# Performance work log

Measured on AMD Instinct MI355X. Metric: run time of the kernel, lower is better.

The kernel has to match this reference:

```python
import jax, jax.numpy as jnp
import numpy as np

B, N, C, L = 32, 1024, 1024, 16  # batch, pixels (HW), channels, visual tokens


def setup_inputs() -> dict:
    key = jax.random.key(0)
    ks = jax.random.split(key, 18)
    s = lambda fan_in: 1.0 / np.sqrt(fan_in)
    def lin(kw, kb, fin, fout):
        W = jax.random.uniform(kw, (fin, fout), jnp.float32, -s(fin), s(fin))
        b = jax.random.uniform(kb, (fout,), jnp.float32, -s(fin), s(fin))
        return W, b
    tok_W, tok_b = lin(ks[0], ks[1], C, L)          # tokenizer pointwise conv
    key_W, key_b = lin(ks[2], ks[3], C, C // 2)     # transformer key proj
    query_W, query_b = lin(ks[4], ks[5], C, C // 2) # transformer query proj
    f1_W, f1_b = lin(ks[6], ks[7], C, C)            # FFN 1
    f2_W, f2_b = lin(ks[8], ks[9], C, C)            # FFN 2
    q_W, q_b = lin(ks[10], ks[11], C, C)            # projector W_q
    k_W, k_b = lin(ks[12], ks[13], C, C)            # projector W_k
    feature_map = jax.random.normal(ks[14], (B, N, C), jnp.float32)
    T_in = jnp.zeros((B, L, C), jnp.float32)  # unused by FilterBasedTokenizer
    return dict(feature_map=feature_map, T_in=T_in,
                tok_W=tok_W, tok_b=tok_b, key_W=key_W, key_b=key_b,
                query_W=query_W, query_b=query_b, f1_W=f1_W, f1_b=f1_b,
                f2_W=f2_W, f2_b=f2_b, q_W=q_W, q_b=q_b, k_W=k_W, k_b=k_b)


def reference(feature_map, T_in, tok_W, tok_b, key_W, key_b, query_W, query_b,
              f1_W, f1_b, f2_W, f2_b, q_W, q_b, k_W, k_b):
    X = feature_map  # [B, N, C]
    # --- FilterBasedTokenizer: softmax over pixel dim, aggregate pixels -> tokens
    proj = X @ tok_W + tok_b                         # [B, N, L]
    attn = jax.nn.softmax(proj, axis=1)              # softmax over N (dim=1)
    T = jnp.einsum('bnl,bnc->blc', attn, X)          # [B, L, C]
    # --- Transformer block on visual tokens
    k = T @ key_W + key_b                            # [B, L, C/2]
    q = T @ query_W + query_b                        # [B, L, C/2]
    scores = jnp.einsum('bld,bmd->blm', k, q)        # [B, L, L]
    T_dash = T + jax.nn.softmax(scores, axis=2) @ T  # self-attn residual
    T_out = T_dash + (jax.nn.relu(T_dash @ f1_W + f1_b) @ f2_W + f2_b)
    # --- Projector: pixels attend to tokens
    sim = jnp.einsum('bnc,blc->bnl', X @ q_W + q_b, T_out @ k_W + k_b)  # [B, N, L]
    X_out = X + jax.nn.softmax(sim, axis=2) @ T_out  # [B, N, C]
    return (X_out, T_out)
```

## Files before the change

kernel.cpp:

```cpp
#include <hip/hip_runtime.h>
#include <hip/hip_bf16.h>
#include <stdint.h>

#define BB 32
#define NN 1024
#define CC 1024
#define LL 16

typedef __attribute__((ext_vector_type(4))) float f32x4;
typedef __attribute__((ext_vector_type(8))) short short8;
typedef __attribute__((ext_vector_type(4))) unsigned short ushort4v;

__device__ __forceinline__ unsigned short f2bf(float f) {
  union { float f; unsigned u; } v; v.f = f;
  unsigned r = v.u + 0x7FFF + ((v.u >> 16) & 1);
  return (unsigned short)(r >> 16);
}
__device__ __forceinline__ float bf2f(unsigned short h) {
  union { unsigned u; float f; } v; v.u = ((unsigned)h) << 16; return v.f;
}
__device__ __forceinline__ short8 cvt8(f32x4 a, f32x4 b) {
  short8 r;
  r[0] = (short)f2bf(a[0]); r[1] = (short)f2bf(a[1]);
  r[2] = (short)f2bf(a[2]); r[3] = (short)f2bf(a[3]);
  r[4] = (short)f2bf(b[0]); r[5] = (short)f2bf(b[1]);
  r[6] = (short)f2bf(b[2]); r[7] = (short)f2bf(b[3]);
  return r;
}

__global__ __launch_bounds__(256) void wprep(
    const float* __restrict__ keyW, const float* __restrict__ queryW,
    const float* __restrict__ f1W, const float* __restrict__ f2W,
    const float* __restrict__ kW, const float* __restrict__ qW,
    const float* __restrict__ tokW, const float* __restrict__ keyb,
    const float* __restrict__ queryb,
    unsigned short* __restrict__ WkqT, unsigned short* __restrict__ f1WT,
    unsigned short* __restrict__ f2WT, unsigned short* __restrict__ kWT,
    unsigned short* __restrict__ qWbf, unsigned short* __restrict__ tokWT,
    float* __restrict__ biaskq)
{
  int z = blockIdx.z;
  int tx = threadIdx.x, ty = threadIdx.y;
  if (z == 5) {
    int gid = (blockIdx.y * 32 + blockIdx.x) * 256 + ty * 32 + tx;
    if (gid < 16384) {
      int l = gid >> 10, c = gid & 1023;
      tokWT[gid] = f2bf(tokW[c * 16 + l]);
    } else if (gid < 17408) {
      int i = gid - 16384;
      biaskq[i] = (i < 512) ? keyb[i] : queryb[i - 512];
    }
    return;
  }
  if (z == 4) {
#pragma unroll
    for (int i = 0; i < 4; ++i) {
      int row = blockIdx.y * 32 + ty + 8 * i;
      int col = blockIdx.x * 32 + tx;
      qWbf[row * 1024 + col] = f2bf(qW[row * 1024 + col]);
    }
    return;
  }
  __shared__ float tile[32][33];
  int j0 = blockIdx.x * 32, k0 = blockIdx.y * 32;
  const float* src = (z == 1) ? f1W : (z == 2) ? f2W : kW;
#pragma unroll
  for (int i = 0; i < 4; ++i) {
    int k = k0 + ty + 8 * i;
    int j = j0 + tx;
    float v;
    if (z == 0) v = (j < 512) ? keyW[k * 512 + j] : queryW[k * 512 + (j - 512)];
    else        v = src[k * 1024 + j];
    tile[ty + 8 * i][tx] = v;
  }
  __syncthreads();
  unsigned short* dst = (z == 0) ? WkqT : (z == 1) ? f1WT : (z == 2) ? f2WT : kWT;
#pragma unroll
  for (int i = 0; i < 4; ++i) {
    int j = j0 + ty + 8 * i;
    dst[j * 1024 + k0 + tx] = f2bf(tile[tx][ty + 8 * i]);
  }
}

__global__ __launch_bounds__(256) void tok_fused(
    const float* __restrict__ X, const unsigned short* __restrict__ tokWT,
    const float* __restrict__ tokB, unsigned short* __restrict__ Tp,
    float* __restrict__ Mloc, float* __restrict__ Sloc)
{
  __shared__ float E[64][16];
  __shared__ float redm[4][16];
  __shared__ float reds[4][16];
  int tid = threadIdx.x, wid = tid >> 6, lane = tid & 63;
  int lr = lane & 15, hi = lane >> 4;
  int b = blockIdx.y, ch = blockIdx.x;
  int pix0 = b * 1024 + ch * 64;
  const float* Ar = X + (size_t)(pix0 + wid * 16 + lr) * 1024 + hi * 8;
  const unsigned short* Br = tokWT + lr * 1024 + hi * 8;
  f32x4 acc = (f32x4)0.f;
#pragma unroll 8
  for (int k0 = 0; k0 < 1024; k0 += 32) {
    f32x4 x0 = *(const f32x4*)(Ar + k0);
    f32x4 x1 = *(const f32x4*)(Ar + k0 + 4);
    short8 bfrag = *(const short8*)(Br + k0);
    acc = __builtin_amdgcn_mfma_f32_16x16x32_bf16(cvt8(x0, x1), bfrag, acc, 0, 0, 0);
  }
  float tb = tokB[lr];
  float sv[4];
#pragma unroll
  for (int rr = 0; rr < 4; ++rr) sv[rr] = acc[rr] + tb;
  float pm = fmaxf(fmaxf(sv[0], sv[1]), fmaxf(sv[2], sv[3]));
  pm = fmaxf(pm, __shfl_xor(pm, 16));
  pm = fmaxf(pm, __shfl_xor(pm, 32));
  if (hi == 0) redm[wid][lr] = pm;
  __syncthreads();
  float m = fmaxf(fmaxf(redm[0][lr], redm[1][lr]), fmaxf(redm[2][lr], redm[3][lr]));
  float ev[4]; float ps = 0.f;
#pragma unroll
  for (int i = 0; i < 4; ++i) { ev[i] = __expf(sv[i] - m); ps += ev[i]; }
  ps += __shfl_xor(ps, 16); ps += __shfl_xor(ps, 32);
  if (hi == 0) reds[wid][lr] = ps;
#pragma unroll
  for (int rr = 0; rr < 4; ++rr)
    E[wid * 16 + hi * 4 + rr][lr] = ev[rr];
  __syncthreads();
  if (tid < 16) {
    float sl = reds[0][tid] + reds[1][tid] + reds[2][tid] + reds[3][tid];
    Mloc[(b * 16 + ch) * 16 + tid] = m;
    Sloc[(b * 16 + ch) * 16 + tid] = sl;
  }
  f32x4 a16[16];
#pragma unroll
  for (int l = 0; l < 16; ++l) a16[l] = (f32x4)0.f;
  const float* xp = X + (size_t)pix0 * 1024 + tid * 4;
  for (int n0 = 0; n0 < 64; n0 += 8) {
    f32x4 xv[8];
#pragma unroll
    for (int i = 0; i < 8; ++i) xv[i] = *(const f32x4*)(xp + (size_t)(n0 + i) * 1024);
#pragma unroll
    for (int i = 0; i < 8; ++i) {
      const f32x4* ar = (const f32x4*)&E[n0 + i][0];
      f32x4 a0 = ar[0], a1 = ar[1], a2 = ar[2], a3 = ar[3];
      f32x4 x0 = xv[i];
      a16[0]  += a0[0]*x0; a16[1]  += a0[1]*x0; a16[2]  += a0[2]*x0; a16[3]  += a0[3]*x0;
      a16[4]  += a1[0]*x0; a16[5]  += a1[1]*x0; a16[6]  += a1[2]*x0; a16[7]  += a1[3]*x0;
      a16[8]  += a2[0]*x0; a16[9]  += a2[1]*x0; a16[10] += a2[2]*x0; a16[11] += a2[3]*x0;
      a16[12] += a3[0]*x0; a16[13] += a3[1]*x0; a16[14] += a3[2]*x0; a16[15] += a3[3]*x0;
    }
  }
  unsigned short* op = Tp + ((size_t)(b * 16 + ch) * 16) * 1024 + tid * 4;
#pragma unroll
  for (int l = 0; l < 16; ++l) {
    f32x4 s = a16[l];
    ushort4v h; h[0]=f2bf(s[0]); h[1]=f2bf(s[1]); h[2]=f2bf(s[2]); h[3]=f2bf(s[3]);
    *(ushort4v*)(op + (size_t)l * 1024) = h;
  }
}

__global__ __launch_bounds__(256) void tmerge(
    const unsigned short* __restrict__ Tp, const float* __restrict__ Mloc,
    const float* __restrict__ Sloc, float* __restrict__ T,
    unsigned short* __restrict__ Tbf)
{
  int tid = threadIdx.x;
  int g = blockIdx.x * 2 + (tid >> 7);
  int b = g >> 4, l = g & 15;
  int j = tid & 127;
  float M = -1e30f;
#pragma unroll
  for (int ch = 0; ch < 16; ++ch) M = fmaxf(M, Mloc[(b * 16 + ch) * 16 + l]);
  float w[16]; float denom = 0.f;
#pragma unroll
  for (int ch = 0; ch < 16; ++ch) {
    w[ch] = __expf(Mloc[(b * 16 + ch) * 16 + l] - M);
    denom += w[ch] * Sloc[(b * 16 + ch) * 16 + l];
  }
  float inv = 1.f / denom;
  float o[8];
#pragma unroll
  for (int t = 0; t < 8; ++t) o[t] = 0.f;
#pragma unroll
  for (int ch = 0; ch < 16; ++ch) {
    const unsigned short* p = Tp + ((size_t)((b * 16 + ch) * 16 + l)) * 1024 + j * 8;
    short8 v = *(const short8*)p;
    float wc = w[ch];
#pragma unroll
    for (int t = 0; t < 8; ++t) o[t] += wc * bf2f((unsigned short)v[t]);
  }
  f32x4 o0, o1; short8 hb;
#pragma unroll
  for (int t = 0; t < 4; ++t) {
    float x0 = o[t] * inv, x1 = o[4 + t] * inv;
    o0[t] = x0; o1[t] = x1;
    hb[t] = (short)f2bf(x0); hb[4 + t] = (short)f2bf(x1);
  }
  *(f32x4*)(T + (size_t)g * 1024 + j * 8) = o0;
  *(f32x4*)(T + (size_t)g * 1024 + j * 8 + 4) = o1;
  *(short8*)(Tbf + (size_t)g * 1024 + j * 8) = hb;
}

template<int RELU, int HAS_BIAS, int HAS_RES, int STORE_F32, int STORE_BF16>
__global__ __launch_bounds__(256) void gemm32x64(
    const unsigned short* __restrict__ A, const unsigned short* __restrict__ Bm,
    const float* __restrict__ bias, const float* __restrict__ res,
    float* __restrict__ outF, unsigned short* __restrict__ outB)
{
  const int K = 1024;
  __shared__ __align__(16) char sh[12288];
  char* Asp = sh;
  char* Bsp = sh + 4096;
  int tid = threadIdx.x, wid = tid >> 6, lane = tid & 63;
  int lr = lane & 15, hi = lane >> 4;
  int m0 = blockIdx.x * 32, n0 = blockIdx.y * 64;
  int arow = tid >> 3, acol = (tid & 7) * 8;
  int brow = tid >> 2, bcol = (tid & 3) * 16;
  const unsigned short* Ap = A + (size_t)(m0 + arow) * K + acol;
  const unsigned short* Bp = Bm + (size_t)(n0 + brow) * K + bcol;
  int aw  = arow * 128 + (((acol * 2) ^ ((arow & 7) << 4)));
  int bw0 = brow * 128 + (((bcol * 2) ^ ((brow & 7) << 4)));
  int bw1 = brow * 128 + ((((bcol * 2) + 16) ^ ((brow & 7) << 4)));
  short8 aR[2]; short8 bR[2][2];
  aR[0]    = *(const short8*)(Ap);
  bR[0][0] = *(const short8*)(Bp);
  bR[0][1] = *(const short8*)(Bp + 8);
  aR[1]    = *(const short8*)(Ap + 64);
  bR[1][0] = *(const short8*)(Bp + 64);
  bR[1][1] = *(const short8*)(Bp + 72);
  f32x4 acc[2];
  acc[0] = (f32x4)0.f; acc[1] = (f32x4)0.f;
  int wm = (wid >> 1) * 16, wn = (wid & 1) * 32;
  int arb = (wm + lr) * 128, arx = ((wm + lr) & 7) << 4;
  for (int s = 0; s < 16; ++s) {
    __syncthreads();
    *(short8*)(Asp + aw)  = aR[s & 1];
    *(short8*)(Bsp + bw0) = bR[s & 1][0];
    *(short8*)(Bsp + bw1) = bR[s & 1][1];
    __syncthreads();
    if (s + 2 < 16) {
      int k0 = (s + 2) * 64;
      aR[s & 1]    = *(const short8*)(Ap + k0);
      bR[s & 1][0] = *(const short8*)(Bp + k0);
      bR[s & 1][1] = *(const short8*)(Bp + k0 + 8);
    }
#pragma unroll
    for (int kk = 0; kk < 2; ++kk) {
      short8 af = *(const short8*)(Asp + arb + (((kk * 64 + hi * 16) ^ arx)));
#pragma unroll
      for (int sn = 0; sn < 2; ++sn) {
        int br = wn + sn * 16 + lr;
        short8 bf = *(const short8*)(Bsp + br * 128 + (((kk * 64 + hi * 16) ^ ((br & 7) << 4))));
        acc[sn] = __builtin_amdgcn_mfma_f32_16x16x32_bf16(af, bf, acc[sn], 0, 0, 0);
      }
    }
  }
  int row0 = m0 + wm + hi * 4;
#pragma unroll
  for (int sn = 0; sn < 2; ++sn) {
    int col = n0 + wn + sn * 16 + lr;
    float bv_ = HAS_BIAS ? bias[col] : 0.f;
#pragma unroll
    for (int rr = 0; rr < 4; ++rr) {
      float x = acc[sn][rr] + bv_;
      if (RELU) x = fmaxf(x, 0.f);
      size_t idx = (size_t)(row0 + rr) * 1024 + col;
      if (HAS_RES) x += res[idx];
      if (STORE_F32) outF[idx] = x;
      if (STORE_BF16) outB[idx] = f2bf(x);
    }
  }
}

__global__ __launch_bounds__(256) void scores_tdash(
    const float* __restrict__ kq, const float* __restrict__ T,
    float* __restrict__ Tdash, unsigned short* __restrict__ Tdbf)
{
  int cs = blockIdx.x, b = blockIdx.y;
  int c0 = cs * 128;
  __shared__ float Ts[16][128];
  int tid = threadIdx.x, lane = tid & 63;
#pragma unroll
  for (int i = 0; i < 2; ++i) {
    int fi = tid + 256 * i;
    int rrow = fi >> 5, c4 = (fi & 31) * 4;
    *(f32x4*)&Ts[rrow][c4] = *(const f32x4*)&T[((size_t)b * 16 + rrow) * 1024 + c0 + c4];
  }
  __syncthreads();
  int l = tid >> 4, m = tid & 15;
  const float* krow = kq + ((size_t)b * 16 + l) * 1024;
  const float* qrow = kq + ((size_t)b * 16 + m) * 1024 + 512;
  float s = 0.f;
#pragma unroll 8
  for (int d = 0; d < 512; d += 4) {
    f32x4 kv = *(const f32x4*)(krow + d);
    f32x4 qv = *(const f32x4*)(qrow + d);
    s += kv[0]*qv[0] + kv[1]*qv[1] + kv[2]*qv[2] + kv[3]*qv[3];
  }
  float mx = s;
  mx = fmaxf(mx, __shfl_xor(mx, 1)); mx = fmaxf(mx, __shfl_xor(mx, 2));
  mx = fmaxf(mx, __shfl_xor(mx, 4)); mx = fmaxf(mx, __shfl_xor(mx, 8));
  float e = __expf(s - mx);
  float sum = e;
  sum += __shfl_xor(sum, 1); sum += __shfl_xor(sum, 2);
  sum += __shfl_xor(sum, 4); sum += __shfl_xor(sum, 8);
  float pv = e / sum;
  float pl[16];
#pragma unroll
  for (int i = 0; i < 16; ++i) pl[i] = __shfl(pv, (lane & 48) + i);
  float* od = Tdash + ((size_t)b * 16 + l) * 1024 + c0;
  unsigned short* ob = Tdbf + ((size_t)b * 16 + l) * 1024 + c0;
#pragma unroll
  for (int h = 0; h < 2; ++h) {
    int c = m * 8 + h * 4;
    f32x4 o = *(const f32x4*)&Ts[l][c];
#pragma unroll
    for (int mm = 0; mm < 16; ++mm) {
      f32x4 tv = *(const f32x4*)&Ts[mm][c];
      o += pl[mm] * tv;
    }
    *(f32x4*)(od + c) = o;
    ushort4v hh; hh[0]=f2bf(o[0]); hh[1]=f2bf(o[1]); hh[2]=f2bf(o[2]); hh[3]=f2bf(o[3]);
    *(ushort4v*)(ob + c) = hh;
  }
}

__global__ __launch_bounds__(256) void r_kernel(
    const unsigned short* __restrict__ Tkbf, const float* __restrict__ qb,
    float* __restrict__ r)
{
  int row = blockIdx.x * 4 + (threadIdx.x >> 6);
  int lane = threadIdx.x & 63;
  const unsigned short* p = Tkbf + (size_t)row * CC;
  float s = 0.f;
#pragma unroll
  for (int h = 0; h < 2; ++h) {
    int d0 = lane * 8 + h * 512;
    short8 v = *(const short8*)&p[d0];
#pragma unroll
    for (int jj = 0; jj < 8; ++jj)
      s += bf2f((unsigned short)v[jj]) * qb[d0 + jj];
  }
#pragma unroll
  for (int msk = 32; msk >= 1; msk >>= 1) s += __shfl_xor(s, msk);
  if (lane == 0) r[row] = s;
}

__global__ __launch_bounds__(256) void sim_out_kernel(
    const float* __restrict__ X, const unsigned short* __restrict__ Gt,
    const float* __restrict__ rbias, const float* __restrict__ Tout,
    float* __restrict__ Xout)
{
  __shared__ float Ps[64][16];
  int tid = threadIdx.x, wid = tid >> 6, lane = tid & 63;
  int lr = lane & 15, hi = lane >> 4;
  int b = blockIdx.y;
  int pix0 = b * 1024 + blockIdx.x * 64;
  const float* Ar = X + (size_t)(pix0 + wid * 16 + lr) * 1024 + hi * 8;
  const unsigned short* Br = Gt + (size_t)b * 16384 + lr * 1024 + hi * 8;
  f32x4 acc = (f32x4)0.f;
#pragma unroll 8
  for (int k0 = 0; k0 < 1024; k0 += 32) {
    f32x4 x0 = *(const f32x4*)(Ar + k0);
    f32x4 x1 = *(const f32x4*)(Ar + k0 + 4);
    short8 bfrag = *(const short8*)(Br + k0);
    acc = __builtin_amdgcn_mfma_f32_16x16x32_bf16(cvt8(x0, x1), bfrag, acc, 0, 0, 0);
  }
  float bv = rbias[b * 16 + lr];
  int prow = wid * 16 + hi * 4;
#pragma unroll
  for (int rr = 0; rr < 4; ++rr) {
    float vv = acc[rr] + bv;
    float mx = vv;
    mx = fmaxf(mx, __shfl_xor(mx, 1)); mx = fmaxf(mx, __shfl_xor(mx, 2));
    mx = fmaxf(mx, __shfl_xor(mx, 4)); mx = fmaxf(mx, __shfl_xor(mx, 8));
    float e = __expf(vv - mx);
    float ss = e;
    ss += __shfl_xor(ss, 1); ss += __shfl_xor(ss, 2);
    ss += __shfl_xor(ss, 4); ss += __shfl_xor(ss, 8);
    Ps[prow + rr][lr] = e / ss;
  }
  __syncthreads();
  int c4 = tid * 4;
  f32x4 tsr[16];
#pragma unroll
  for (int l = 0; l < 16; ++l)
    tsr[l] = *(const f32x4*)&Tout[((size_t)b * 16 + l) * 1024 + c4];
  const float* xp = X + (size_t)pix0 * 1024 + c4;
  float* op = Xout + (size_t)pix0 * 1024 + c4;
#pragma unroll 2
  for (int n = 0; n < 64; ++n) {
    f32x4 xv = *(const f32x4*)(xp + (size_t)n * 1024);
    const f32x4* pr = (const f32x4*)&Ps[n][0];
    f32x4 p0 = pr[0], p1 = pr[1], p2 = pr[2], p3 = pr[3];
    f32x4 o = xv;
    o += p0[0]*tsr[0];  o += p0[1]*tsr[1];  o += p0[2]*tsr[2];  o += p0[3]*tsr[3];
    o += p1[0]*tsr[4];  o += p1[1]*tsr[5];  o += p1[2]*tsr[6];  o += p1[3]*tsr[7];
    o += p2[0]*tsr[8];  o += p2[1]*tsr[9];  o += p2[2]*tsr[10]; o += p2[3]*tsr[11];
    o += p3[0]*tsr[12]; o += p3[1]*tsr[13]; o += p3[2]*tsr[14]; o += p3[3]*tsr[15];
    __builtin_nontemporal_store(o, (f32x4*)(op + (size_t)n * 1024));
  }
}

extern "C" void kernel_launch(void* const* d_in, const int* in_sizes, int n_in,
                              void* d_out, int out_size, void* d_ws, size_t ws_size,
                              hipStream_t stream)
{
  const float* X      = (const float*)d_in[0];
  const float* tokW   = (const float*)d_in[2];
  const float* tokB   = (const float*)d_in[3];
  const float* keyW   = (const float*)d_in[4];
  const float* keyB   = (const float*)d_in[5];
  const float* queryW = (const float*)d_in[6];
  const float* queryB = (const float*)d_in[7];
  const float* f1W    = (const float*)d_in[8];
  const float* f1B    = (const float*)d_in[9];
  const float* f2W    = (const float*)d_in[10];
  const float* f2B    = (const float*)d_in[11];
  const float* qW     = (const float*)d_in[12];
  const float* qB     = (const float*)d_in[13];
  const float* kW     = (const float*)d_in[14];
  const float* kB     = (const float*)d_in[15];

  float* Xout = (float*)d_out;
  float* Tout = (float*)d_out + (size_t)BB * NN * CC;

  char* ws = (char*)d_ws;
  size_t off = 0;
  auto alloc_f = [&](size_t n) { float* pp = (float*)(ws + off); off += n * 4; return pp; };
  float* Tbuf   = alloc_f(524288);
  float* kqbuf  = alloc_f(524288);
  float* Tdash  = alloc_f(524288);
  float* rbuf   = alloc_f(1024);
  float* biaskq = alloc_f(1024);
  float* Mloc   = alloc_f(8192);
  float* Sloc   = alloc_f(8192);
  auto alloc_h = [&](size_t n) { unsigned short* pp = (unsigned short*)(ws + off); off += n * 2; return pp; };
  unsigned short* Tp     = alloc_h(8388608);
  unsigned short* Tbf    = alloc_h(524288);
  unsigned short* Tdbf   = alloc_h(524288);
  unsigned short* Hbf    = alloc_h(524288);
  unsigned short* Toutbf = alloc_h(524288);
  unsigned short* Tkbf   = alloc_h(524288);
  unsigned short* Gtbf   = alloc_h(524288);
  unsigned short* WkqT   = alloc_h(1048576);
  unsigned short* f1WT   = alloc_h(1048576);
  unsigned short* f2WT   = alloc_h(1048576);
  unsigned short* kWT    = alloc_h(1048576);
  unsigned short* qWbf   = alloc_h(1048576);
  unsigned short* tokWT  = alloc_h(16384);
  (void)ws_size; (void)in_sizes; (void)n_in; (void)out_size;

  wprep<<<dim3(32, 32, 6), dim3(32, 8), 0, stream>>>(keyW, queryW, f1W, f2W, kW, qW,
                                                     tokW, keyB, queryB,
                                                     WkqT, f1WT, f2WT, kWT, qWbf, tokWT, biaskq);
  tok_fused<<<dim3(16, 32), 256, 0, stream>>>(X, tokWT, tokB, Tp, Mloc, Sloc);
  tmerge<<<256, 256, 0, stream>>>(Tp, Mloc, Sloc, Tbuf, Tbf);
  gemm32x64<0,1,0,1,0><<<dim3(16, 16), 256, 0, stream>>>(Tbf, WkqT, biaskq, nullptr, kqbuf, nullptr);
  scores_tdash<<<dim3(8, 32), 256, 0, stream>>>(kqbuf, Tbuf, Tdash, Tdbf);
  gemm32x64<1,1,0,0,1><<<dim3(16, 16), 256, 0, stream>>>(Tdbf, f1WT, f1B, nullptr, nullptr, Hbf);
  gemm32x64<0,1,1,1,1><<<dim3(16, 16), 256, 0, stream>>>(Hbf, f2WT, f2B, Tdash, Tout, Toutbf);
  gemm32x64<0,1,0,0,1><<<dim3(16, 16), 256, 0, stream>>>(Toutbf, kWT, kB, nullptr, nullptr, Tkbf);
  r_kernel<<<128, 256, 0, stream>>>(Tkbf, qB, rbuf);
  gemm32x64<0,0,0,0,1><<<dim3(16, 16), 256, 0, stream>>>(Tkbf, qWbf, nullptr, nullptr, nullptr, Gtbf);
  sim_out_kernel<<<dim3(16, 32), 256, 0, stream>>>(X, Gtbf, rbuf, Tout, Xout);
}
```

Before: 175.9 us.

## Fuse token-transformer chain into one cooperative kernel and overlap weight prep

Replaces the sequence of small kernels (tmerge, five GEMMs, scores, r) with a single cooperative kernel of 256 blocks that uses grid-wide syncs between stages, removing per-launch gaps. The weight transpose and bf16 conversion moves into extra blocks of tok_fused so it runs alongside the tokenizer pass over X. The GEMM register prefetch depth also goes from 2 to 4 stages. Grid syncs have their own cost, and cooperative launch requires all 256 blocks to be resident at once.

```diff
diff --git a/kernel.cpp b/kernel.cpp
--- a/kernel.cpp
+++ b/kernel.cpp
@@ -1,6 +1,9 @@
 #include <hip/hip_runtime.h>
 #include <hip/hip_bf16.h>
+#include <hip/hip_cooperative_groups.h>
 #include <stdint.h>
+
+namespace cg = cooperative_groups;
 
 #define BB 32
 #define NN 1024
@@ -28,69 +31,74 @@
   return r;
 }
 
-__global__ __launch_bounds__(256) void wprep(
+__global__ __launch_bounds__(256) void tokprep(
+    const float* __restrict__ tokW, const float* __restrict__ keyb,
+    const float* __restrict__ queryb,
+    unsigned short* __restrict__ tokWT, float* __restrict__ biaskq)
+{
+  int gid = blockIdx.x * 256 + threadIdx.x;
+  if (gid < 16384) {
+    int l = gid >> 10, c = gid & 1023;
+    tokWT[gid] = f2bf(tokW[c * 16 + l]);
+  } else if (gid < 17408) {
+    int i = gid - 16384;
+    biaskq[i] = (i < 512) ? keyb[i] : queryb[i - 512];
+  }
+}
+
+__global__ __launch_bounds__(256) void tok_fused(
+    const float* __restrict__ X, const unsigned short* __restrict__ tokWT,
+    const float* __restrict__ tokB, unsigned short* __restrict__ Tp,
+    float* __restrict__ Mloc, float* __restrict__ Sloc,
     const float* __restrict__ keyW, const float* __restrict__ queryW,
     const float* __restrict__ f1W, const float* __restrict__ f2W,
     const float* __restrict__ kW, const float* __restrict__ qW,
-    const float* __restrict__ tokW, const float* __restrict__ keyb,
-    const float* __restrict__ queryb,
     unsigned short* __restrict__ WkqT, unsigned short* __restrict__ f1WT,
     unsigned short* __restrict__ f2WT, unsigned short* __restrict__ kWT,
-    unsigned short* __restrict__ qWbf, unsigned short* __restrict__ tokWT,
-    float* __restrict__ biaskq)
+    unsigned short* __restrict__ qWbf)
 {
-  int z = blockIdx.z;
-  int tx = threadIdx.x, ty = threadIdx.y;
-  if (z == 5) {
-    int gid = (blockIdx.y * 32 + blockIdx.x) * 256 + ty * 32 + tx;
-    if (gid < 16384) {
-      int l = gid >> 10, c = gid & 1023;
-      tokWT[gid] = f2bf(tokW[c * 16 + l]);
-    } else if (gid < 17408) {
-      int i = gid - 16384;
-      biaskq[i] = (i < 512) ? keyb[i] : queryb[i - 512];
+  __shared__ __align__(16) char shbuf[4608];
+  int tid = threadIdx.x;
+  if (blockIdx.x >= 16) {
+    int prep_id = (blockIdx.x - 16) * 32 + blockIdx.y;
+    int tx = tid & 31, ty = tid >> 5;
+    float (*tile)[33] = (float(*)[33])shbuf;
+    for (int i = 0; i < 32; ++i) {
+      int t = prep_id * 32 + i;
+      int z = t >> 10, idx = t & 1023;
+      int j0 = (idx & 31) * 32, k0 = (idx >> 5) * 32;
+      if (z == 4) {
+#pragma unroll
+        for (int q = 0; q < 4; ++q) {
+          int row = k0 + ty + 8 * q, col = j0 + tx;
+          qWbf[row * 1024 + col] = f2bf(qW[row * 1024 + col]);
+        }
+      } else {
+        const float* src = (z == 1) ? f1W : (z == 2) ? f2W : kW;
+#pragma unroll
+        for (int q = 0; q < 4; ++q) {
+          int k = k0 + ty + 8 * q, j = j0 + tx;
+          float v;
+          if (z == 0) v = (j < 512) ? keyW[k * 512 + j] : queryW[k * 512 + (j - 512)];
+          else        v = src[k * 1024 + j];
+          tile[ty + 8 * q][tx] = v;
+        }
+        __syncthreads();
+        unsigned short* dst = (z == 0) ? WkqT : (z == 1) ? f1WT : (z == 2) ? f2WT : kWT;
+#pragma unroll
+        for (int q = 0; q < 4; ++q) {
+          int j = j0 + ty + 8 * q;
+          dst[j * 1024 + k0 + tx] = f2bf(tile[tx][ty + 8 * q]);
+        }
+        __syncthreads();
+      }
     }
     return;
   }
-  if (z == 4) {
-#pragma unroll
-    for (int i = 0; i < 4; ++i) {
-      int row = blockIdx.y * 32 + ty + 8 * i;
-      int col = blockIdx.x * 32 + tx;
-      qWbf[row * 1024 + col] = f2bf(qW[row * 1024 + col]);
-    }
-    return;
-  }
-  __shared__ float tile[32][33];
-  int j0 = blockIdx.x * 32, k0 = blockIdx.y * 32;
-  const float* src = (z == 1) ? f1W : (z == 2) ? f2W : kW;
-#pragma unroll
-  for (int i = 0; i < 4; ++i) {
-    int k = k0 + ty + 8 * i;
-    int j = j0 + tx;
-    float v;
-    if (z == 0) v = (j < 512) ? keyW[k * 512 + j] : queryW[k * 512 + (j - 512)];
-    else        v = src[k * 1024 + j];
-    tile[ty + 8 * i][tx] = v;
-  }
-  __syncthreads();
-  unsigned short* dst = (z == 0) ? WkqT : (z == 1) ? f1WT : (z == 2) ? f2WT : kWT;
-#pragma unroll
-  for (int i = 0; i < 4; ++i) {
-    int j = j0 + ty + 8 * i;
-    dst[j * 1024 + k0 + tx] = f2bf(tile[tx][ty + 8 * i]);
-  }
-}
-
-__global__ __launch_bounds__(256) void tok_fused(
-    const float* __restrict__ X, const unsigned short* __restrict__ tokWT,
-    const float* __restrict__ tokB, unsigned short* __restrict__ Tp,
-    float* __restrict__ Mloc, float* __restrict__ Sloc)
-{
-  __shared__ float E[64][16];
-  __shared__ float redm[4][16];
-  __shared__ float reds[4][16];
-  int tid = threadIdx.x, wid = tid >> 6, lane = tid & 63;
+  float (*E)[16] = (float(*)[16])shbuf;
+  float (*redm)[16] = (float(*)[16])(shbuf + 4096);
+  float (*reds)[16] = (float(*)[16])(shbuf + 4352);
+  int wid = tid >> 6, lane = tid & 63;
   int lr = lane & 15, hi = lane >> 4;
   int b = blockIdx.y, ch = blockIdx.x;
   int pix0 = b * 1024 + ch * 64;
@@ -156,23 +164,31 @@
   }
 }
 
-__global__ __launch_bounds__(256) void tmerge(
-    const unsigned short* __restrict__ Tp, const float* __restrict__ Mloc,
-    const float* __restrict__ Sloc, float* __restrict__ T,
-    unsigned short* __restrict__ Tbf)
-{
+struct ChainArgs {
+  const unsigned short* Tp; const float* Mloc; const float* Sloc;
+  float* Tbuf; unsigned short* Tbf;
+  const unsigned short* WkqT; const float* biaskq; float* kqbuf;
+  float* Tdash; unsigned short* Tdbf;
+  const unsigned short* f1WT; const float* f1B; unsigned short* Hbf;
+  const unsigned short* f2WT; const float* f2B; float* Tout; unsigned short* Toutbf;
+  const unsigned short* kWT; const float* kB; unsigned short* Tkbf;
+  const unsigned short* qWbf; const float* qB; float* rbuf;
+  unsigned short* Gtbf;
+};
+
+__device__ __forceinline__ void tmerge_stage(int bid, const ChainArgs& a) {
   int tid = threadIdx.x;
-  int g = blockIdx.x * 2 + (tid >> 7);
+  int g = bid * 2 + (tid >> 7);
   int b = g >> 4, l = g & 15;
   int j = tid & 127;
   float M = -1e30f;
 #pragma unroll
-  for (int ch = 0; ch < 16; ++ch) M = fmaxf(M, Mloc[(b * 16 + ch) * 16 + l]);
+  for (int ch = 0; ch < 16; ++ch) M = fmaxf(M, a.Mloc[(b * 16 + ch) * 16 + l]);
   float w[16]; float denom = 0.f;
 #pragma unroll
   for (int ch = 0; ch < 16; ++ch) {
-    w[ch] = __expf(Mloc[(b * 16 + ch) * 16 + l] - M);
-    denom += w[ch] * Sloc[(b * 16 + ch) * 16 + l];
+    w[ch] = __expf(a.Mloc[(b * 16 + ch) * 16 + l] - M);
+    denom += w[ch] * a.Sloc[(b * 16 + ch) * 16 + l];
   }
   float inv = 1.f / denom;
   float o[8];
@@ -180,7 +196,7 @@
   for (int t = 0; t < 8; ++t) o[t] = 0.f;
 #pragma unroll
   for (int ch = 0; ch < 16; ++ch) {
-    const unsigned short* p = Tp + ((size_t)((b * 16 + ch) * 16 + l)) * 1024 + j * 8;
+    const unsigned short* p = a.Tp + ((size_t)((b * 16 + ch) * 16 + l)) * 1024 + j * 8;
     short8 v = *(const short8*)p;
     float wc = w[ch];
 #pragma unroll
@@ -193,24 +209,22 @@
     o0[t] = x0; o1[t] = x1;
     hb[t] = (short)f2bf(x0); hb[4 + t] = (short)f2bf(x1);
   }
-  *(f32x4*)(T + (size_t)g * 1024 + j * 8) = o0;
-  *(f32x4*)(T + (size_t)g * 1024 + j * 8 + 4) = o1;
-  *(short8*)(Tbf + (size_t)g * 1024 + j * 8) = hb;
+  *(f32x4*)(a.Tbuf + (size_t)g * 1024 + j * 8) = o0;
+  *(f32x4*)(a.Tbuf + (size_t)g * 1024 + j * 8 + 4) = o1;
+  *(short8*)(a.Tbf + (size_t)g * 1024 + j * 8) = hb;
 }
 
 template<int RELU, int HAS_BIAS, int HAS_RES, int STORE_F32, int STORE_BF16>
-__global__ __launch_bounds__(256) void gemm32x64(
-    const unsigned short* __restrict__ A, const unsigned short* __restrict__ Bm,
-    const float* __restrict__ bias, const float* __restrict__ res,
-    float* __restrict__ outF, unsigned short* __restrict__ outB)
+__device__ __forceinline__ void gemm_stage(int bid, char* smem,
+    const unsigned short* A, const unsigned short* Bm,
+    const float* bias, const float* res, float* outF, unsigned short* outB)
 {
   const int K = 1024;
-  __shared__ __align__(16) char sh[12288];
-  char* Asp = sh;
-  char* Bsp = sh + 4096;
+  char* Asp = smem;
+  char* Bsp = smem + 4096;
   int tid = threadIdx.x, wid = tid >> 6, lane = tid & 63;
   int lr = lane & 15, hi = lane >> 4;
-  int m0 = blockIdx.x * 32, n0 = blockIdx.y * 64;
+  int m0 = (bid & 15) * 32, n0 = (bid >> 4) * 64;
   int arow = tid >> 3, acol = (tid & 7) * 8;
   int brow = tid >> 2, bcol = (tid & 3) * 16;
   const unsigned short* Ap = A + (size_t)(m0 + arow) * K + acol;
@@ -218,28 +232,28 @@
   int aw  = arow * 128 + (((acol * 2) ^ ((arow & 7) << 4)));
   int bw0 = brow * 128 + (((bcol * 2) ^ ((brow & 7) << 4)));
   int bw1 = brow * 128 + ((((bcol * 2) + 16) ^ ((brow & 7) << 4)));
-  short8 aR[2]; short8 bR[2][2];
-  aR[0]    = *(const short8*)(Ap);
-  bR[0][0] = *(const short8*)(Bp);
-  bR[0][1] = *(const short8*)(Bp + 8);
-  aR[1]    = *(const short8*)(Ap + 64);
-  bR[1][0] = *(const short8*)(Bp + 64);
-  bR[1][1] = *(const short8*)(Bp + 72);
+  short8 aR[4]; short8 bR[4][2];
+#pragma unroll
+  for (int p = 0; p < 4; ++p) {
+    aR[p]    = *(const short8*)(Ap + p * 64);
+    bR[p][0] = *(const short8*)(Bp + p * 64);
+    bR[p][1] = *(const short8*)(Bp + p * 64 + 8);
+  }
   f32x4 acc[2];
   acc[0] = (f32x4)0.f; acc[1] = (f32x4)0.f;
   int wm = (wid >> 1) * 16, wn = (wid & 1) * 32;
   int arb = (wm + lr) * 128, arx = ((wm + lr) & 7) << 4;
   for (int s = 0; s < 16; ++s) {
     __syncthreads();
-    *(short8*)(Asp + aw)  = aR[s & 1];
-    *(short8*)(Bsp + bw0) = bR[s & 1][0];
-    *(short8*)(Bsp + bw1) = bR[s & 1][1];
+    *(short8*)(Asp + aw)  = aR[s & 3];
+    *(short8*)(Bsp + bw0) = bR[s & 3][0];
+    *(short8*)(Bsp + bw1) = bR[s & 3][1];
     __syncthreads();
-    if (s + 2 < 16) {
-      int k0 = (s + 2) * 64;
-      aR[s & 1]    = *(const short8*)(Ap + k0);
-      bR[s & 1][0] = *(const short8*)(Bp + k0);
-      bR[s & 1][1] = *(const short8*)(Bp + k0 + 8);
+    if (s + 4 < 16) {
+      int k0 = (s + 4) * 64;
+      aR[s & 3]    = *(const short8*)(Ap + k0);
+      bR[s & 3][0] = *(const short8*)(Bp + k0);
+      bR[s & 3][1] = *(const short8*)(Bp + k0 + 8);
     }
 #pragma unroll
     for (int kk = 0; kk < 2; ++kk) {
@@ -269,24 +283,21 @@
   }
 }
 
-__global__ __launch_bounds__(256) void scores_tdash(
-    const float* __restrict__ kq, const float* __restrict__ T,
-    float* __restrict__ Tdash, unsigned short* __restrict__ Tdbf)
-{
-  int cs = blockIdx.x, b = blockIdx.y;
+__device__ __forceinline__ void scores_stage(int bid, char* smem, const ChainArgs& a) {
+  float (*Ts)[128] = (float(*)[128])smem;
+  int cs = bid & 7, b = bid >> 3;
   int c0 = cs * 128;
-  __shared__ float Ts[16][128];
   int tid = threadIdx.x, lane = tid & 63;
 #pragma unroll
   for (int i = 0; i < 2; ++i) {
     int fi = tid + 256 * i;
     int rrow = fi >> 5, c4 = (fi & 31) * 4;
-    *(f32x4*)&Ts[rrow][c4] = *(const f32x4*)&T[((size_t)b * 16 + rrow) * 1024 + c0 + c4];
+    *(f32x4*)&Ts[rrow][c4] = *(const f32x4*)&a.Tbuf[((size_t)b * 16 + rrow) * 1024 + c0 + c4];
   }
   __syncthreads();
   int l = tid >> 4, m = tid & 15;
-  const float* krow = kq + ((size_t)b * 16 + l) * 1024;
-  const float* qrow = kq + ((size_t)b * 16 + m) * 1024 + 512;
+  const float* krow = a.kqbuf + ((size_t)b * 16 + l) * 1024;
+  const float* qrow = a.kqbuf + ((size_t)b * 16 + m) * 1024 + 512;
   float s = 0.f;
 #pragma unroll 8
   for (int d = 0; d < 512; d += 4) {
@@ -305,8 +316,8 @@
   float pl[16];
 #pragma unroll
   for (int i = 0; i < 16; ++i) pl[i] = __shfl(pv, (lane & 48) + i);
-  float* od = Tdash + ((size_t)b * 16 + l) * 1024 + c0;
-  unsigned short* ob = Tdbf + ((size_t)b * 16 + l) * 1024 + c0;
+  float* od = a.Tdash + ((size_t)b * 16 + l) * 1024 + c0;
+  unsigned short* ob = a.Tdbf + ((size_t)b * 16 + l) * 1024 + c0;
 #pragma unroll
   for (int h = 0; h < 2; ++h) {
     int c = m * 8 + h * 4;
@@ -322,25 +333,44 @@
   }
 }
 
-__global__ __launch_bounds__(256) void r_kernel(
-    const unsigned short* __restrict__ Tkbf, const float* __restrict__ qb,
-    float* __restrict__ r)
-{
-  int row = blockIdx.x * 4 + (threadIdx.x >> 6);
-  int lane = threadIdx.x & 63;
-  const unsigned short* p = Tkbf + (size_t)row * CC;
-  float s = 0.f;
-#pragma unroll
-  for (int h = 0; h < 2; ++h) {
-    int d0 = lane * 8 + h * 512;
-    short8 v = *(const short8*)&p[d0];
-#pragma unroll
-    for (int jj = 0; jj < 8; ++jj)
-      s += bf2f((unsigned short)v[jj]) * qb[d0 + jj];
-  }
-#pragma unroll
-  for (int msk = 32; msk >= 1; msk >>= 1) s += __shfl_xor(s, msk);
-  if (lane == 0) r[row] = s;
+__device__ __forceinline__ void r_stage(int bid, const ChainArgs& a) {
+  int tid = threadIdx.x, wid = tid >> 6, lane = tid & 63;
+#pragma unroll
+  for (int rw = 0; rw < 8; ++rw) {
+    int m = bid * 32 + wid * 8 + rw;
+    const unsigned short* p = a.Tkbf + (size_t)m * 1024 + lane * 16;
+    short8 v0 = *(const short8*)p;
+    short8 v1 = *(const short8*)(p + 8);
+    float s = 0.f;
+#pragma unroll
+    for (int j = 0; j < 8; ++j) {
+      s += bf2f((unsigned short)v0[j]) * a.qB[lane * 16 + j];
+      s += bf2f((unsigned short)v1[j]) * a.qB[lane * 16 + 8 + j];
+    }
+#pragma unroll
+    for (int msk = 32; msk >= 1; msk >>= 1) s += __shfl_xor(s, msk);
+    if (lane == 0) a.rbuf[m] = s;
+  }
+}
+
+__global__ __launch_bounds__(256) void chain_kernel(ChainArgs a) {
+  cg::grid_group gg = cg::this_grid();
+  __shared__ __align__(16) char smem[12288];
+  int bid = blockIdx.x;
+  tmerge_stage(bid, a);
+  gg.sync();
+  gemm_stage<0,1,0,1,0>(bid, smem, a.Tbf, a.WkqT, a.biaskq, nullptr, a.kqbuf, nullptr);
+  gg.sync();
+  scores_stage(bid, smem, a);
+  gg.sync();
+  gemm_stage<1,1,0,0,1>(bid, smem, a.Tdbf, a.f1WT, a.f1B, nullptr, nullptr, a.Hbf);
+  gg.sync();
+  gemm_stage<0,1,1,1,1>(bid, smem, a.Hbf, a.f2WT, a.f2B, a.Tdash, a.Tout, a.Toutbf);
+  gg.sync();
+  gemm_stage<0,1,0,0,1>(bid, smem, a.Toutbf, a.kWT, a.kB, nullptr, nullptr, a.Tkbf);
+  gg.sync();
+  gemm_stage<0,0,0,0,1>(bid, smem, a.Tkbf, a.qWbf, nullptr, nullptr, nullptr, a.Gtbf);
+  if (bid < 16) r_stage(bid, a);
 }
 
 __global__ __launch_bounds__(256) void sim_out_kernel(
@@ -448,17 +478,23 @@
   unsigned short* tokWT  = alloc_h(16384);
   (void)ws_size; (void)in_sizes; (void)n_in; (void)out_size;
 
-  wprep<<<dim3(32, 32, 6), dim3(32, 8), 0, stream>>>(keyW, queryW, f1W, f2W, kW, qW,
-                                                     tokW, keyB, queryB,
-                                                     WkqT, f1WT, f2WT, kWT, qWbf, tokWT, biaskq);
-  tok_fused<<<dim3(16, 32), 256, 0, stream>>>(X, tokWT, tokB, Tp, Mloc, Sloc);
-  tmerge<<<256, 256, 0, stream>>>(Tp, Mloc, Sloc, Tbuf, Tbf);
-  gemm32x64<0,1,0,1,0><<<dim3(16, 16), 256, 0, stream>>>(Tbf, WkqT, biaskq, nullptr, kqbuf, nullptr);
-  scores_tdash<<<dim3(8, 32), 256, 0, stream>>>(kqbuf, Tbuf, Tdash, Tdbf);
-  gemm32x64<1,1,0,0,1><<<dim3(16, 16), 256, 0, stream>>>(Tdbf, f1WT, f1B, nullptr, nullptr, Hbf);
-  gemm32x64<0,1,1,1,1><<<dim3(16, 16), 256, 0, stream>>>(Hbf, f2WT, f2B, Tdash, Tout, Toutbf);
-  gemm32x64<0,1,0,0,1><<<dim3(16, 16), 256, 0, stream>>>(Toutbf, kWT, kB, nullptr, nullptr, Tkbf);
-  r_kernel<<<128, 256, 0, stream>>>(Tkbf, qB, rbuf);
-  gemm32x64<0,0,0,0,1><<<dim3(16, 16), 256, 0, stream>>>(Tkbf, qWbf, nullptr, nullptr, nullptr, Gtbf);
+  tokprep<<<68, 256, 0, stream>>>(tokW, keyB, queryB, tokWT, biaskq);
+  tok_fused<<<dim3(21, 32), 256, 0, stream>>>(X, tokWT, tokB, Tp, Mloc, Sloc,
+                                              keyW, queryW, f1W, f2W, kW, qW,
+                                              WkqT, f1WT, f2WT, kWT, qWbf);
+
+  ChainArgs ca;
+  ca.Tp = Tp; ca.Mloc = Mloc; ca.Sloc = Sloc;
+  ca.Tbuf = Tbuf; ca.Tbf = Tbf;
+  ca.WkqT = WkqT; ca.biaskq = biaskq; ca.kqbuf = kqbuf;
+  ca.Tdash = Tdash; ca.Tdbf = Tdbf;
+  ca.f1WT = f1WT; ca.f1B = f1B; ca.Hbf = Hbf;
+  ca.f2WT = f2WT; ca.f2B = f2B; ca.Tout = Tout; ca.Toutbf = Toutbf;
+  ca.kWT = kWT; ca.kB = kB; ca.Tkbf = Tkbf;
+  ca.qWbf = qWbf; ca.qB = qB; ca.rbuf = rbuf;
+  ca.Gtbf = Gtbf;
+  void* kp[] = { &ca };
+  hipLaunchCooperativeKernel((void*)chain_kernel, dim3(256), dim3(256), kp, 0, stream);
+
   sim_out_kernel<<<dim3(16, 32), 256, 0, stream>>>(X, Gtbf, rbuf, Tout, Xout);
 }
```

New measurement: 402.4 us. +128.8%, slower.

## Fold weight prep into tokenizer kernel, split K across 512-thread blocks, deepen GEMM prefetch

Applied to the files above, without the earlier changes.

The weight transpose/convert work moves from a separate kernel into extra blocks of the tokenizer launch, so it overlaps with the X-reading tokenizer. A small tokprep kernel keeps the tokWT and bias setup. The tokenizer and sim_out kernels now use 512 threads and split the K-reduction between two wave groups, combined through shared memory, to get more parallelism per block. The small GEMM's register prefetch goes from 2 to 4 stages. In exchange there are more registers, an extra sync, and prep blocks that each loop over 32 tiles.

```diff
diff --git a/kernel.cpp b/kernel.cpp
--- a/kernel.cpp
+++ b/kernel.cpp
@@ -8,8 +8,10 @@
 #define LL 16
 
 typedef __attribute__((ext_vector_type(4))) float f32x4;
+typedef __attribute__((ext_vector_type(2))) float f32x2;
 typedef __attribute__((ext_vector_type(8))) short short8;
 typedef __attribute__((ext_vector_type(4))) unsigned short ushort4v;
+typedef __attribute__((ext_vector_type(2))) unsigned short ushort2v;
 
 __device__ __forceinline__ unsigned short f2bf(float f) {
   union { float f; unsigned u; } v; v.f = f;
@@ -28,131 +30,146 @@
   return r;
 }
 
-__global__ __launch_bounds__(256) void wprep(
+__global__ __launch_bounds__(256) void tokprep(
+    const float* __restrict__ tokW, const float* __restrict__ keyb,
+    const float* __restrict__ queryb,
+    unsigned short* __restrict__ tokWT, float* __restrict__ biaskq)
+{
+  int gid = blockIdx.x * 256 + threadIdx.x;
+  if (gid < 16384) {
+    int l = gid >> 10, c = gid & 1023;
+    tokWT[gid] = f2bf(tokW[c * 16 + l]);
+  } else if (gid < 17408) {
+    int i = gid - 16384;
+    biaskq[i] = (i < 512) ? keyb[i] : queryb[i - 512];
+  }
+}
+
+__global__ __launch_bounds__(512) void tok_fused(
+    const float* __restrict__ X, const unsigned short* __restrict__ tokWT,
+    const float* __restrict__ tokB, unsigned short* __restrict__ Tp,
+    float* __restrict__ Mloc, float* __restrict__ Sloc,
     const float* __restrict__ keyW, const float* __restrict__ queryW,
     const float* __restrict__ f1W, const float* __restrict__ f2W,
     const float* __restrict__ kW, const float* __restrict__ qW,
-    const float* __restrict__ tokW, const float* __restrict__ keyb,
-    const float* __restrict__ queryb,
     unsigned short* __restrict__ WkqT, unsigned short* __restrict__ f1WT,
     unsigned short* __restrict__ f2WT, unsigned short* __restrict__ kWT,
-    unsigned short* __restrict__ qWbf, unsigned short* __restrict__ tokWT,
-    float* __restrict__ biaskq)
-{
-  int z = blockIdx.z;
-  int tx = threadIdx.x, ty = threadIdx.y;
-  if (z == 5) {
-    int gid = (blockIdx.y * 32 + blockIdx.x) * 256 + ty * 32 + tx;
-    if (gid < 16384) {
-      int l = gid >> 10, c = gid & 1023;
-      tokWT[gid] = f2bf(tokW[c * 16 + l]);
-    } else if (gid < 17408) {
-      int i = gid - 16384;
-      biaskq[i] = (i < 512) ? keyb[i] : queryb[i - 512];
+    unsigned short* __restrict__ qWbf)
+{
+  __shared__ float E[64][16];
+  __shared__ __align__(16) f32x4 accbuf[4][64];
+  __shared__ float redm[4][16], reds[4][16];
+  int tid = threadIdx.x;
+  if (blockIdx.x >= 16) {
+    int prep_id = (blockIdx.x - 16) * 32 + blockIdx.y;
+    int tx = tid & 31, ty = tid >> 5;
+    __shared__ float tile[32][33];
+    for (int i = 0; i < 32; ++i) {
+      int t = prep_id * 32 + i;
+      int z = t >> 10, idx = t & 1023;
+      int j0 = (idx & 31) * 32, k0 = (idx >> 5) * 32;
+      if (z == 4) {
+#pragma unroll
+        for (int q = 0; q < 2; ++q) {
+          int row = k0 + ty + 16 * q, col = j0 + tx;
+          qWbf[row * 1024 + col] = f2bf(qW[row * 1024 + col]);
+        }
+      } else {
+        const float* src = (z == 1) ? f1W : (z == 2) ? f2W : kW;
+#pragma unroll
+        for (int q = 0; q < 2; ++q) {
+          int k = k0 + ty + 16 * q, j = j0 + tx;
+          float v;
+          if (z == 0) v = (j < 512) ? keyW[k * 512 + j] : queryW[k * 512 + (j - 512)];
+          else        v = src[k * 1024 + j];
+          tile[ty + 16 * q][tx] = v;
+        }
+        __syncthreads();
+        unsigned short* dst = (z == 0) ? WkqT : (z == 1) ? f1WT : (z == 2) ? f2WT : kWT;
+#pragma unroll
+        for (int q = 0; q < 2; ++q) {
+          int j = j0 + ty + 16 * q;
+          dst[j * 1024 + k0 + tx] = f2bf(tile[tx][ty + 16 * q]);
+        }
+        __syncthreads();
+      }
     }
     return;
   }
-  if (z == 4) {
-#pragma unroll
-    for (int i = 0; i < 4; ++i) {
-      int row = blockIdx.y * 32 + ty + 8 * i;
-      int col = blockIdx.x * 32 + tx;
-      qWbf[row * 1024 + col] = f2bf(qW[row * 1024 + col]);
-    }
-    return;
-  }
-  __shared__ float tile[32][33];
-  int j0 = blockIdx.x * 32, k0 = blockIdx.y * 32;
-  const float* src = (z == 1) ? f1W : (z == 2) ? f2W : kW;
-#pragma unroll
-  for (int i = 0; i < 4; ++i) {
-    int k = k0 + ty + 8 * i;
-    int j = j0 + tx;
-    float v;
-    if (z == 0) v = (j < 512) ? keyW[k * 512 + j] : queryW[k * 512 + (j - 512)];
-    else        v = src[k * 1024 + j];
-    tile[ty + 8 * i][tx] = v;
-  }
-  __syncthreads();
-  unsigned short* dst = (z == 0) ? WkqT : (z == 1) ? f1WT : (z == 2) ? f2WT : kWT;
-#pragma unroll
-  for (int i = 0; i < 4; ++i) {
-    int j = j0 + ty + 8 * i;
-    dst[j * 1024 + k0 + tx] = f2bf(tile[tx][ty + 8 * i]);
-  }
-}
-
-__global__ __launch_bounds__(256) void tok_fused(
-    const float* __restrict__ X, const unsigned short* __restrict__ tokWT,
-    const float* __restrict__ tokB, unsigned short* __restrict__ Tp,
-    float* __restrict__ Mloc, float* __restrict__ Sloc)
-{
-  __shared__ float E[64][16];
-  __shared__ float redm[4][16];
-  __shared__ float reds[4][16];
-  int tid = threadIdx.x, wid = tid >> 6, lane = tid & 63;
+  int wid = tid >> 6, lane = tid & 63;
   int lr = lane & 15, hi = lane >> 4;
+  int rowgrp = wid & 3, khalf = wid >> 2;
   int b = blockIdx.y, ch = blockIdx.x;
   int pix0 = b * 1024 + ch * 64;
-  const float* Ar = X + (size_t)(pix0 + wid * 16 + lr) * 1024 + hi * 8;
-  const unsigned short* Br = tokWT + lr * 1024 + hi * 8;
+  const float* Ar = X + (size_t)(pix0 + rowgrp * 16 + lr) * 1024 + khalf * 512 + hi * 8;
+  const unsigned short* Br = tokWT + lr * 1024 + khalf * 512 + hi * 8;
   f32x4 acc = (f32x4)0.f;
 #pragma unroll 8
-  for (int k0 = 0; k0 < 1024; k0 += 32) {
+  for (int k0 = 0; k0 < 512; k0 += 32) {
     f32x4 x0 = *(const f32x4*)(Ar + k0);
     f32x4 x1 = *(const f32x4*)(Ar + k0 + 4);
     short8 bfrag = *(const short8*)(Br + k0);
     acc = __builtin_amdgcn_mfma_f32_16x16x32_bf16(cvt8(x0, x1), bfrag, acc, 0, 0, 0);
   }
+  if (khalf == 1) accbuf[rowgrp][lane] = acc;
+  __syncthreads();
   float tb = tokB[lr];
   float sv[4];
-#pragma unroll
-  for (int rr = 0; rr < 4; ++rr) sv[rr] = acc[rr] + tb;
-  float pm = fmaxf(fmaxf(sv[0], sv[1]), fmaxf(sv[2], sv[3]));
-  pm = fmaxf(pm, __shfl_xor(pm, 16));
-  pm = fmaxf(pm, __shfl_xor(pm, 32));
-  if (hi == 0) redm[wid][lr] = pm;
-  __syncthreads();
-  float m = fmaxf(fmaxf(redm[0][lr], redm[1][lr]), fmaxf(redm[2][lr], redm[3][lr]));
-  float ev[4]; float ps = 0.f;
-#pragma unroll
-  for (int i = 0; i < 4; ++i) { ev[i] = __expf(sv[i] - m); ps += ev[i]; }
-  ps += __shfl_xor(ps, 16); ps += __shfl_xor(ps, 32);
-  if (hi == 0) reds[wid][lr] = ps;
-#pragma unroll
-  for (int rr = 0; rr < 4; ++rr)
-    E[wid * 16 + hi * 4 + rr][lr] = ev[rr];
+  if (khalf == 0) {
+    f32x4 other = accbuf[rowgrp][lane];
+#pragma unroll
+    for (int rr = 0; rr < 4; ++rr) sv[rr] = acc[rr] + other[rr] + tb;
+    float pm = fmaxf(fmaxf(sv[0], sv[1]), fmaxf(sv[2], sv[3]));
+    pm = fmaxf(pm, __shfl_xor(pm, 16));
+    pm = fmaxf(pm, __shfl_xor(pm, 32));
+    if (hi == 0) redm[rowgrp][lr] = pm;
+  }
+  __syncthreads();
+  if (khalf == 0) {
+    float m = fmaxf(fmaxf(redm[0][lr], redm[1][lr]), fmaxf(redm[2][lr], redm[3][lr]));
+    float ev[4]; float ps = 0.f;
+#pragma unroll
+    for (int i = 0; i < 4; ++i) { ev[i] = __expf(sv[i] - m); ps += ev[i]; }
+    ps += __shfl_xor(ps, 16); ps += __shfl_xor(ps, 32);
+    if (hi == 0) reds[rowgrp][lr] = ps;
+#pragma unroll
+    for (int rr = 0; rr < 4; ++rr)
+      E[rowgrp * 16 + hi * 4 + rr][lr] = ev[rr];
+    if (wid == 0 && hi == 0) {
+    }
+  }
   __syncthreads();
   if (tid < 16) {
+    float m2 = fmaxf(fmaxf(redm[0][tid], redm[1][tid]), fmaxf(redm[2][tid], redm[3][tid]));
     float sl = reds[0][tid] + reds[1][tid] + reds[2][tid] + reds[3][tid];
-    Mloc[(b * 16 + ch) * 16 + tid] = m;
+    Mloc[(b * 16 + ch) * 16 + tid] = m2;
     Sloc[(b * 16 + ch) * 16 + tid] = sl;
   }
-  f32x4 a16[16];
-#pragma unroll
-  for (int l = 0; l < 16; ++l) a16[l] = (f32x4)0.f;
-  const float* xp = X + (size_t)pix0 * 1024 + tid * 4;
+  f32x2 a16[16];
+#pragma unroll
+  for (int l = 0; l < 16; ++l) a16[l] = (f32x2)0.f;
+  const float* xp = X + (size_t)pix0 * 1024 + tid * 2;
   for (int n0 = 0; n0 < 64; n0 += 8) {
-    f32x4 xv[8];
-#pragma unroll
-    for (int i = 0; i < 8; ++i) xv[i] = *(const f32x4*)(xp + (size_t)(n0 + i) * 1024);
+    f32x2 xv[8];
+#pragma unroll
+    for (int i = 0; i < 8; ++i) xv[i] = *(const f32x2*)(xp + (size_t)(n0 + i) * 1024);
 #pragma unroll
     for (int i = 0; i < 8; ++i) {
       const f32x4* ar = (const f32x4*)&E[n0 + i][0];
       f32x4 a0 = ar[0], a1 = ar[1], a2 = ar[2], a3 = ar[3];
-      f32x4 x0 = xv[i];
+      f32x2 x0 = xv[i];
       a16[0]  += a0[0]*x0; a16[1]  += a0[1]*x0; a16[2]  += a0[2]*x0; a16[3]  += a0[3]*x0;
       a16[4]  += a1[0]*x0; a16[5]  += a1[1]*x0; a16[6]  += a1[2]*x0; a16[7]  += a1[3]*x0;
       a16[8]  += a2[0]*x0; a16[9]  += a2[1]*x0; a16[10] += a2[2]*x0; a16[11] += a2[3]*x0;
       a16[12] += a3[0]*x0; a16[13] += a3[1]*x0; a16[14] += a3[2]*x0; a16[15] += a3[3]*x0;
     }
   }
-  unsigned short* op = Tp + ((size_t)(b * 16 + ch) * 16) * 1024 + tid * 4;
+  unsigned short* op = Tp + ((size_t)(b * 16 + ch) * 16) * 1024 + tid * 2;
 #pragma unroll
   for (int l = 0; l < 16; ++l) {
-    f32x4 s = a16[l];
-    ushort4v h; h[0]=f2bf(s[0]); h[1]=f2bf(s[1]); h[2]=f2bf(s[2]); h[3]=f2bf(s[3]);
-    *(ushort4v*)(op + (size_t)l * 1024) = h;
+    f32x2 s = a16[l];
+    ushort2v h; h[0] = f2bf(s[0]); h[1] = f2bf(s[1]);
+    *(ushort2v*)(op + (size_t)l * 1024) = h;
   }
 }
 
@@ -218,28 +235,28 @@
   int aw  = arow * 128 + (((acol * 2) ^ ((arow & 7) << 4)));
   int bw0 = brow * 128 + (((bcol * 2) ^ ((brow & 7) << 4)));
   int bw1 = brow * 128 + ((((bcol * 2) + 16) ^ ((brow & 7) << 4)));
-  short8 aR[2]; short8 bR[2][2];
-  aR[0]    = *(const short8*)(Ap);
-  bR[0][0] = *(const short8*)(Bp);
-  bR[0][1] = *(const short8*)(Bp + 8);
-  aR[1]    = *(const short8*)(Ap + 64);
-  bR[1][0] = *(const short8*)(Bp + 64);
-  bR[1][1] = *(const short8*)(Bp + 72);
+  short8 aR[4]; short8 bR[4][2];
+#pragma unroll
+  for (int p = 0; p < 4; ++p) {
+    aR[p]    = *(const short8*)(Ap + p * 64);
+    bR[p][0] = *(const short8*)(Bp + p * 64);
+    bR[p][1] = *(const short8*)(Bp + p * 64 + 8);
+  }
   f32x4 acc[2];
   acc[0] = (f32x4)0.f; acc[1] = (f32x4)0.f;
   int wm = (wid >> 1) * 16, wn = (wid & 1) * 32;
   int arb = (wm + lr) * 128, arx = ((wm + lr) & 7) << 4;
   for (int s = 0; s < 16; ++s) {
     __syncthreads();
-    *(short8*)(Asp + aw)  = aR[s & 1];
-    *(short8*)(Bsp + bw0) = bR[s & 1][0];
-    *(short8*)(Bsp + bw1) = bR[s & 1][1];
+    *(short8*)(Asp + aw)  = aR[s & 3];
+    *(short8*)(Bsp + bw0) = bR[s & 3][0];
+    *(short8*)(Bsp + bw1) = bR[s & 3][1];
     __syncthreads();
-    if (s + 2 < 16) {
-      int k0 = (s + 2) * 64;
-      aR[s & 1]    = *(const short8*)(Ap + k0);
-      bR[s & 1][0] = *(const short8*)(Bp + k0);
-      bR[s & 1][1] = *(const short8*)(Bp + k0 + 8);
+    if (s + 4 < 16) {
+      int k0 = (s + 4) * 64;
+      aR[s & 3]    = *(const short8*)(Ap + k0);
+      bR[s & 3][0] = *(const short8*)(Bp + k0);
+      bR[s & 3][1] = *(const short8*)(Bp + k0 + 8);
     }
 #pragma unroll
     for (int kk = 0; kk < 2; ++kk) {
@@ -343,52 +360,60 @@
   if (lane == 0) r[row] = s;
 }
 
-__global__ __launch_bounds__(256) void sim_out_kernel(
+__global__ __launch_bounds__(512) void sim_out_kernel(
     const float* __restrict__ X, const unsigned short* __restrict__ Gt,
     const float* __restrict__ rbias, const float* __restrict__ Tout,
     float* __restrict__ Xout)
 {
   __shared__ float Ps[64][16];
+  __shared__ __align__(16) f32x4 accbuf[4][64];
   int tid = threadIdx.x, wid = tid >> 6, lane = tid & 63;
   int lr = lane & 15, hi = lane >> 4;
+  int rowgrp = wid & 3, khalf = wid >> 2;
   int b = blockIdx.y;
   int pix0 = b * 1024 + blockIdx.x * 64;
-  const float* Ar = X + (size_t)(pix0 + wid * 16 + lr) * 1024 + hi * 8;
-  const unsigned short* Br = Gt + (size_t)b * 16384 + lr * 1024 + hi * 8;
+  const float* Ar = X + (size_t)(pix0 + rowgrp * 16 + lr) * 1024 + khalf * 512 + hi * 8;
+  const unsigned short* Br = Gt + (size_t)b * 16384 + lr * 1024 + khalf * 512 + hi * 8;
   f32x4 acc = (f32x4)0.f;
 #pragma unroll 8
-  for (int k0 = 0; k0 < 1024; k0 += 32) {
+  for (int k0 = 0; k0 < 512; k0 += 32) {
     f32x4 x0 = *(const f32x4*)(Ar + k0);
     f32x4 x1 = *(const f32x4*)(Ar + k0 + 4);
     short8 bfrag = *(const short8*)(Br + k0);
     acc = __builtin_amdgcn_mfma_f32_16x16x32_bf16(cvt8(x0, x1), bfrag, acc, 0, 0, 0);
   }
-  float bv = rbias[b * 16 + lr];
-  int prow = wid * 16 + hi * 4;
-#pragma unroll
-  for (int rr = 0; rr < 4; ++rr) {
-    float vv = acc[rr] + bv;
-    float mx = vv;
-    mx = fmaxf(mx, __shfl_xor(mx, 1)); mx = fmaxf(mx, __shfl_xor(mx, 2));
-    mx = fmaxf(mx, __shfl_xor(mx, 4)); mx = fmaxf(mx, __shfl_xor(mx, 8));
-    float e = __expf(vv - mx);
-    float ss = e;
-    ss += __shfl_xor(ss, 1); ss += __shfl_xor(ss, 2);
-    ss += __shfl_xor(ss, 4); ss += __shfl_xor(ss, 8);
-    Ps[prow + rr][lr] = e / ss;
-  }
-  __syncthreads();
-  int c4 = tid * 4;
+  if (khalf == 1) accbuf[rowgrp][lane] = acc;
+  __syncthreads();
+  if (khalf == 0) {
+    f32x4 other = accbuf[rowgrp][lane];
+    float bv = rbias[b * 16 + lr];
+    int prow = rowgrp * 16 + hi * 4;
+#pragma unroll
+    for (int rr = 0; rr < 4; ++rr) {
+      float vv = acc[rr] + other[rr] + bv;
+      float mx = vv;
+      mx = fmaxf(mx, __shfl_xor(mx, 1)); mx = fmaxf(mx, __shfl_xor(mx, 2));
+      mx = fmaxf(mx, __shfl_xor(mx, 4)); mx = fmaxf(mx, __shfl_xor(mx, 8));
+      float e = __expf(vv - mx);
+      float ss = e;
+      ss += __shfl_xor(ss, 1); ss += __shfl_xor(ss, 2);
+      ss += __shfl_xor(ss, 4); ss += __shfl_xor(ss, 8);
+      Ps[prow + rr][lr] = e / ss;
+    }
+  }
+  __syncthreads();
+  int half = tid >> 8, tn = tid & 255;
+  int c4 = tn * 4;
   f32x4 tsr[16];
 #pragma unroll
   for (int l = 0; l < 16; ++l)
     tsr[l] = *(const f32x4*)&Tout[((size_t)b * 16 + l) * 1024 + c4];
-  const float* xp = X + (size_t)pix0 * 1024 + c4;
-  float* op = Xout + (size_t)pix0 * 1024 + c4;
+  const float* xp = X + (size_t)(pix0 + half * 32) * 1024 + c4;
+  float* op = Xout + (size_t)(pix0 + half * 32) * 1024 + c4;
 #pragma unroll 2
-  for (int n = 0; n < 64; ++n) {
+  for (int n = 0; n < 32; ++n) {
     f32x4 xv = *(const f32x4*)(xp + (size_t)n * 1024);
-    const f32x4* pr = (const f32x4*)&Ps[n][0];
+    const f32x4* pr = (const f32x4*)&Ps[half * 32 + n][0];
     f32x4 p0 = pr[0], p1 = pr[1], p2 = pr[2], p3 = pr[3];
     f32x4 o = xv;
     o += p0[0]*tsr[0];  o += p0[1]*tsr[1];  o += p0[2]*tsr[2];  o += p0[3]*tsr[3];
@@ -448,10 +473,10 @@
   unsigned short* tokWT  = alloc_h(16384);
   (void)ws_size; (void)in_sizes; (void)n_in; (void)out_size;
 
-  wprep<<<dim3(32, 32, 6), dim3(32, 8), 0, stream>>>(keyW, queryW, f1W, f2W, kW, qW,
-                                                     tokW, keyB, queryB,
-                                                     WkqT, f1WT, f2WT, kWT, qWbf, tokWT, biaskq);
-  tok_fused<<<dim3(16, 32), 256, 0, stream>>>(X, tokWT, tokB, Tp, Mloc, Sloc);
+  tokprep<<<68, 256, 0, stream>>>(tokW, keyB, queryB, tokWT, biaskq);
+  tok_fused<<<dim3(21, 32), 512, 0, stream>>>(X, tokWT, tokB, Tp, Mloc, Sloc,
+                                              keyW, queryW, f1W, f2W, kW, qW,
+                                              WkqT, f1WT, f2WT, kWT, qWbf);
   tmerge<<<256, 256, 0, stream>>>(Tp, Mloc, Sloc, Tbuf, Tbf);
   gemm32x64<0,1,0,1,0><<<dim3(16, 16), 256, 0, stream>>>(Tbf, WkqT, biaskq, nullptr, kqbuf, nullptr);
   scores_tdash<<<dim3(8, 32), 256, 0, stream>>>(kqbuf, Tbuf, Tdash, Tdbf);
@@ -460,5 +485,5 @@
   gemm32x64<0,1,0,0,1><<<dim3(16, 16), 256, 0, stream>>>(Toutbf, kWT, kB, nullptr, nullptr, Tkbf);
   r_kernel<<<128, 256, 0, stream>>>(Tkbf, qB, rbuf);
   gemm32x64<0,0,0,0,1><<<dim3(16, 16), 256, 0, stream>>>(Tkbf, qWbf, nullptr, nullptr, nullptr, Gtbf);
-  sim_out_kernel<<<dim3(16, 32), 256, 0, stream>>>(X, Gtbf, rbuf, Tout, Xout);
-}
+  sim_out_kernel<<<dim3(16, 32), 512, 0, stream>>>(X, Gtbf, rbuf, Tout, Xout);
+}
```

Result: slower. 185.7 us (+5.6%).
